# Kernel tuning notes

Measured on AMD Instinct MI355X. Metric: run time of the kernel, lower is better.

## Reference

```python
import jax
import jax.numpy as jnp
import numpy as np
from jax import lax

B, T, D = 32, 256, 512   # batch, seq len, controller_dim (== memory_dim)
S = 2048                 # memory_slots
EPS_LN = 1e-5            # nn.LayerNorm default eps
EPS_NRM = 1e-12          # F.normalize default eps


def setup_inputs() -> dict:
    key = jax.random.key(0)
    ks = jax.random.split(key, 12)
    sc = 1.0 / np.sqrt(D)  # roughly torch Linear init scale
    return {
        "controller_seq": jax.random.normal(ks[0], (B, T, D), dtype=jnp.float32),
        "memory": jax.random.normal(ks[1], (S, D), dtype=jnp.float32),
        "Wk": jax.random.normal(ks[2], (D, D), dtype=jnp.float32) * sc,
        "bk": jax.random.normal(ks[3], (D,), dtype=jnp.float32) * sc,
        "We": jax.random.normal(ks[4], (D, D), dtype=jnp.float32) * sc,
        "be": jax.random.normal(ks[5], (D,), dtype=jnp.float32) * sc,
        "Ww": jax.random.normal(ks[6], (D, D), dtype=jnp.float32) * sc,
        "bw": jax.random.normal(ks[7], (D,), dtype=jnp.float32) * sc,
        "Wg": jax.random.normal(ks[8], (D, D), dtype=jnp.float32) * sc,
        "bg": jax.random.normal(ks[9], (D,), dtype=jnp.float32) * sc,
        "gamma": jnp.ones((D,), dtype=jnp.float32),
        "beta": jnp.zeros((D,), dtype=jnp.float32),
    }


def _l2norm(x, axis=-1):
    # matches F.normalize: x / max(||x||, eps)
    n = jnp.sqrt(jnp.sum(x * x, axis=axis, keepdims=True))
    return x / jnp.maximum(n, EPS_NRM)


def _layernorm(x, gamma, beta):
    mu = jnp.mean(x, axis=-1, keepdims=True)
    var = jnp.mean((x - mu) ** 2, axis=-1, keepdims=True)
    return (x - mu) * lax.rsqrt(var + EPS_LN) * gamma + beta


def reference(controller_seq, memory, Wk, bk, We, be, Ww, bw, Wg, bg, gamma, beta):
    batch = controller_seq.shape[0]

    def step(mem, c):  # mem: [S, Dm], c: [B, Dc]
        # --- read (addressing by cosine similarity) ---
        k = c @ Wk.T + bk                       # [B, Dm]
        sim = _l2norm(k) @ _l2norm(mem).T       # [B, S]
        w = jax.nn.softmax(sim, axis=-1)        # [B, S]
        read_val = w @ mem                      # [B, Dm]
        # --- write (erase / add, averaged over batch) ---
        erase = jax.nn.sigmoid(c @ We.T + be)   # [B, Dm]
        add = c @ Ww.T + bw                     # [B, Dm]
        # mean_b (1 - w_bs * e_bd) = 1 - (w^T e)/B ; avoids [B,S,Dm] intermediate
        erase_m = 1.0 - jnp.einsum("bs,bd->sd", w, erase) / batch
        add_m = jnp.einsum("bs,bd->sd", w, add) / batch
        new_mem = _layernorm(mem * erase_m + add_m, gamma, beta)  # dropout in eval mode
        # --- gated output ---
        g = jax.nn.sigmoid(c @ Wg.T + bg)       # [B, Dm]
        out_t = g * c + (1.0 - g) * read_val
        return new_mem, out_t

    _, outs = lax.scan(step, memory, jnp.swapaxes(controller_seq, 0, 1))  # outs: [T, B, D]
    return jnp.swapaxes(outs, 0, 1)  # [B, T, D]
```

## Files before the change

### kernel.cpp

```cpp
#include <hip/hip_runtime.h>

#define DEV __device__ __forceinline__

namespace {
constexpr int Bc = 32;
constexpr int Tc = 256;
constexpr int Dc = 512;
constexpr int Sc = 2048;
constexpr int NBLK = 256;
constexpr int NW   = 128;
constexpr int ROWS = Sc / NW;

constexpr size_t OFF_KN  = 0;
constexpr size_t OFF_E   = OFF_KN  + (size_t)Tc * Bc * Dc;
constexpr size_t OFF_A   = OFF_E   + (size_t)Tc * Bc * Dc;
constexpr size_t OFF_MEM = OFF_A   + (size_t)Tc * Bc * Dc;
constexpr size_t OFF_EW  = OFF_MEM + (size_t)2 * Sc * Dc;
constexpr size_t OFF_RP  = OFF_EW  + (size_t)2 * Sc * Bc;
constexpr size_t OFF_DEN = OFF_RP  + (size_t)2 * 16 * Bc * Dc;
constexpr size_t OFF_CNT = OFF_DEN + (size_t)Tc * Bc;
}

DEV float sigm(float x) { return 1.0f / (1.0f + __expf(-x)); }

DEV float ld1cg(const float* p) {
  unsigned u = __hip_atomic_load((const unsigned*)p, __ATOMIC_RELAXED,
                                 __HIP_MEMORY_SCOPE_AGENT);
  return __uint_as_float(u);
}
DEV void st1cg(float* p, float v) {
  __hip_atomic_store((unsigned*)p, __float_as_uint(v), __ATOMIC_RELAXED,
                     __HIP_MEMORY_SCOPE_AGENT);
}
DEV float2 ld2cg(const float* p) {
  unsigned long long u = __hip_atomic_load((const unsigned long long*)p,
                                           __ATOMIC_RELAXED, __HIP_MEMORY_SCOPE_AGENT);
  union { unsigned long long u; float2 f; } c; c.u = u; return c.f;
}
DEV void st2cg(float* p, float2 v) {
  union { float2 f; unsigned long long u; } c; c.f = v;
  __hip_atomic_store((unsigned long long*)p, c.u, __ATOMIC_RELAXED,
                     __HIP_MEMORY_SCOPE_AGENT);
}

__global__ __launch_bounds__(256) void k_gemm(
    const float* __restrict__ A,
    const float* __restrict__ Wk, const float* __restrict__ bk,
    const float* __restrict__ We, const float* __restrict__ be,
    const float* __restrict__ Ww, const float* __restrict__ bw,
    const float* __restrict__ Wg, const float* __restrict__ bg,
    float* __restrict__ ws, float* __restrict__ gout)
{
  __shared__ float As[32][68];
  __shared__ float Bs[32][68];

  const int bid = blockIdx.x;
  const int mat = bid >> 10;
  const int rem = bid & 1023;
  const int rt = rem >> 3, jt = rem & 7;
  const int rbase = rt * 64, jbase = jt * 64;

  const float* Wm; const float* bm;
  if      (mat == 0) { Wm = Wk; bm = bk; }
  else if (mat == 1) { Wm = We; bm = be; }
  else if (mat == 2) { Wm = Ww; bm = bw; }
  else               { Wm = Wg; bm = bg; }

  const int tid = threadIdx.x;
  const int lr = tid >> 2;
  const int lk = (tid & 3) * 8;
  const int ty = tid >> 4, tx = tid & 15;

  float acc[4][4] = {};

  for (int k0 = 0; k0 < Dc; k0 += 32) {
    const float4 a0 = *(const float4*)&A [(size_t)(rbase + lr) * Dc + k0 + lk];
    const float4 a1 = *(const float4*)&A [(size_t)(rbase + lr) * Dc + k0 + lk + 4];
    const float4 b0 = *(const float4*)&Wm[(size_t)(jbase + lr) * Dc + k0 + lk];
    const float4 b1 = *(const float4*)&Wm[(size_t)(jbase + lr) * Dc + k0 + lk + 4];
    __syncthreads();
    As[lk + 0][lr] = a0.x; As[lk + 1][lr] = a0.y; As[lk + 2][lr] = a0.z; As[lk + 3][lr] = a0.w;
    As[lk + 4][lr] = a1.x; As[lk + 5][lr] = a1.y; As[lk + 6][lr] = a1.z; As[lk + 7][lr] = a1.w;
    Bs[lk + 0][lr] = b0.x; Bs[lk + 1][lr] = b0.y; Bs[lk + 2][lr] = b0.z; Bs[lk + 3][lr] = b0.w;
    Bs[lk + 4][lr] = b1.x; Bs[lk + 5][lr] = b1.y; Bs[lk + 6][lr] = b1.z; Bs[lk + 7][lr] = b1.w;
    __syncthreads();
    #pragma unroll
    for (int kk = 0; kk < 32; ++kk) {
      const float4 av = *(const float4*)&As[kk][ty * 4];
      const float4 bv = *(const float4*)&Bs[kk][tx * 4];
      const float ar[4] = {av.x, av.y, av.z, av.w};
      const float br[4] = {bv.x, bv.y, bv.z, bv.w};
      #pragma unroll
      for (int i = 0; i < 4; ++i)
        #pragma unroll
        for (int j = 0; j < 4; ++j)
          acc[i][j] = fmaf(ar[i], br[j], acc[i][j]);
    }
  }

  const float4 bias = *(const float4*)&bm[jbase + tx * 4];
  const float bi[4] = {bias.x, bias.y, bias.z, bias.w};
  #pragma unroll
  for (int i = 0; i < 4; ++i) {
    const int r = rbase + ty * 4 + i;
    float v[4];
    #pragma unroll
    for (int j = 0; j < 4; ++j) {
      v[j] = acc[i][j] + bi[j];
      if (mat & 1) v[j] = sigm(v[j]);
    }
    float4 o; o.x = v[0]; o.y = v[1]; o.z = v[2]; o.w = v[3];
    if (mat == 3) {
      *(float4*)&gout[(size_t)r * Dc + jbase + tx * 4] = o;
    } else {
      float* dst = ws + (mat == 0 ? OFF_KN : (mat == 1 ? OFF_E : OFF_A));
      const int t = r & 255, b = r >> 8;
      *(float4*)&dst[((size_t)t * Bc + b) * Dc + jbase + tx * 4] = o;
    }
  }
}

__global__ __launch_bounds__(256) void k_knorm(float* __restrict__ kn)
{
  const int row = blockIdx.x * 4 + (threadIdx.x >> 6);
  const int lane = threadIdx.x & 63;
  float* p = kn + (size_t)row * Dc;
  float4 v0 = *(const float4*)&p[lane * 4];
  float4 v1 = *(const float4*)&p[256 + lane * 4];
  float ss = v0.x*v0.x + v0.y*v0.y + v0.z*v0.z + v0.w*v0.w
           + v1.x*v1.x + v1.y*v1.y + v1.z*v1.z + v1.w*v1.w;
  #pragma unroll
  for (int off = 32; off >= 1; off >>= 1) ss += __shfl_xor(ss, off);
  const float inv = 1.0f / fmaxf(sqrtf(ss), 1e-12f);
  v0.x *= inv; v0.y *= inv; v0.z *= inv; v0.w *= inv;
  v1.x *= inv; v1.y *= inv; v1.z *= inv; v1.w *= inv;
  *(float4*)&p[lane * 4] = v0;
  *(float4*)&p[256 + lane * 4] = v1;
}

DEV void sim_phase(const float* __restrict__ knp, float* __restrict__ ewn,
                   float* __restrict__ denp, float (*xb)[516],
                   const float* invn_s, float* sred, int s0, int tid)
{
  const int r = tid >> 4, bp = tid & 15;
  const float* k0p = knp + (size_t)bp * Dc;
  const float* k1p = knp + (size_t)(bp + 16) * Dc;
  float acc0 = 0.f, acc1 = 0.f;
  #pragma unroll 4
  for (int dq = 0; dq < Dc / 4; ++dq) {
    const float4 y4 = *(const float4*)&xb[r][dq * 4];
    const float4 ka = *(const float4*)&k0p[dq * 4];
    const float4 kb = *(const float4*)&k1p[dq * 4];
    acc0 = fmaf(y4.x, ka.x, acc0); acc0 = fmaf(y4.y, ka.y, acc0);
    acc0 = fmaf(y4.z, ka.z, acc0); acc0 = fmaf(y4.w, ka.w, acc0);
    acc1 = fmaf(y4.x, kb.x, acc1); acc1 = fmaf(y4.y, kb.y, acc1);
    acc1 = fmaf(y4.z, kb.z, acc1); acc1 = fmaf(y4.w, kb.w, acc1);
  }
  const float iv = invn_s[r];
  const float e0 = __expf(acc0 * iv);
  const float e1 = __expf(acc1 * iv);
  st1cg(&ewn[(size_t)(s0 + r) * Bc + bp], e0);
  st1cg(&ewn[(size_t)(s0 + r) * Bc + bp + 16], e1);
  if (tid < 32) sred[tid] = 0.f;
  __syncthreads();
  atomicAdd(&sred[bp], e0);
  atomicAdd(&sred[bp + 16], e1);
  __syncthreads();
  if (tid < 32) atomicAdd(&denp[tid], sred[tid]);
}

__global__ __launch_bounds__(256) void k_prologue(
    const float* __restrict__ mem_in, float* __restrict__ ws)
{
  __shared__ float xbuf[16][516];
  __shared__ float sred[32];
  __shared__ float invn_s[16];

  float* kn   = ws + OFF_KN;
  float* memb = ws + OFF_MEM;
  float* ewb  = ws + OFF_EW;
  float* den  = ws + OFF_DEN;

  const int bid = blockIdx.x, tid = threadIdx.x;
  const int s0 = bid * ROWS;
  const int c0 = tid * 2;
  #pragma unroll
  for (int r = 0; r < ROWS; ++r) {
    const float2 m = *(const float2*)&mem_in[(size_t)(s0 + r) * Dc + c0];
    *(float2*)&xbuf[r][c0] = m;
    st2cg(&memb[(size_t)(s0 + r) * Dc + c0], m);
  }
  __syncthreads();
  {
    const int row = tid >> 4, li = tid & 15;
    float ss = 0.f;
    #pragma unroll
    for (int i = 0; i < 8; ++i) {
      const float4 v = *(const float4*)&xbuf[row][(li + i * 16) * 4];
      ss += v.x*v.x + v.y*v.y + v.z*v.z + v.w*v.w;
    }
    ss += __shfl_xor(ss, 8); ss += __shfl_xor(ss, 4);
    ss += __shfl_xor(ss, 2); ss += __shfl_xor(ss, 1);
    if (li == 0) invn_s[row] = 1.0f / fmaxf(sqrtf(ss), 1e-12f);
  }
  __syncthreads();
  sim_phase(kn, ewb, den, xbuf, invn_s, sred, s0, tid);
}

DEV void gbar(unsigned* cnt, unsigned target)
{
  __syncthreads();
  if (threadIdx.x == 0) {
    __hip_atomic_fetch_add(cnt, 1u, __ATOMIC_RELAXED, __HIP_MEMORY_SCOPE_AGENT);
    unsigned v = __hip_atomic_load(cnt, __ATOMIC_RELAXED, __HIP_MEMORY_SCOPE_AGENT);
    while (v < target) {
      __builtin_amdgcn_s_sleep(2);
      v = __hip_atomic_load(cnt, __ATOMIC_RELAXED, __HIP_MEMORY_SCOPE_AGENT);
    }
  }
  __syncthreads();
}

__global__ __launch_bounds__(256) void k_main(
    const float* __restrict__ cs,
    const float* __restrict__ gamma, const float* __restrict__ beta,
    float* __restrict__ ws, float* __restrict__ out)
{
  __shared__ float xbuf[16][516];
  __shared__ float wbuf[16][32];
  __shared__ float sred[32];
  __shared__ float mu_s[16], rs_s[16], invn_s[16];
  __shared__ float dinv_s[32];

  float* kn   = ws + OFF_KN;
  float* eptb = ws + OFF_E;
  float* aptb = ws + OFF_A;
  float* memb = ws + OFF_MEM;
  float* ewb  = ws + OFF_EW;
  float* rp   = ws + OFF_RP;
  float* den  = ws + OFF_DEN;
  unsigned* cnt = (unsigned*)(ws + OFF_CNT);

  const int bid = blockIdx.x, tid = threadIdx.x;
  const float inv32 = 1.0f / 32.0f;
  unsigned bart = 0;

  for (int t = 0; t <= Tc; ++t) {
    if (bid < NW) {
      if (t < Tc - 1) {
        const int s0 = bid * ROWS;
        const int c0 = tid * 2;
        const float* ewc = ewb + (size_t)(t & 1) * Sc * Bc;
        float*       ewn = ewb + (size_t)((t + 1) & 1) * Sc * Bc;
        const float* memc = memb + (size_t)(t & 1) * Sc * Dc;
        float*       memn = memb + (size_t)((t + 1) & 1) * Sc * Dc;

        if (tid < 32) dinv_s[tid] = 1.0f / ld1cg(&den[(size_t)t * Bc + tid]);
        __syncthreads();
        for (int idx = tid; idx < ROWS * 32; idx += 256) {
          const int r = idx >> 5, b = idx & 31;
          wbuf[r][b] = ld1cg(&ewc[(size_t)(s0 + r) * Bc + b]) * dinv_s[b];
        }
        __syncthreads();

        float2 er[ROWS] = {}, ad[ROWS] = {};
        const float* ept = eptb + (size_t)t * Bc * Dc;
        const float* apt = aptb + (size_t)t * Bc * Dc;
        #pragma unroll 4
        for (int b = 0; b < 32; ++b) {
          const float2 ev = *(const float2*)&ept[(size_t)b * Dc + c0];
          const float2 av = *(const float2*)&apt[(size_t)b * Dc + c0];
          #pragma unroll
          for (int r = 0; r < ROWS; ++r) {
            const float wv = wbuf[r][b];
            er[r].x = fmaf(wv, ev.x, er[r].x); er[r].y = fmaf(wv, ev.y, er[r].y);
            ad[r].x = fmaf(wv, av.x, ad[r].x); ad[r].y = fmaf(wv, av.y, ad[r].y);
          }
        }
        float2 xr[ROWS];
        #pragma unroll
        for (int r = 0; r < ROWS; ++r) {
          const float2 m = ld2cg(&memc[(size_t)(s0 + r) * Dc + c0]);
          float2 x;
          x.x = m.x * (1.0f - er[r].x * inv32) + ad[r].x * inv32;
          x.y = m.y * (1.0f - er[r].y * inv32) + ad[r].y * inv32;
          xr[r] = x;
          *(float2*)&xbuf[r][c0] = x;
        }
        __syncthreads();
        {
          const int row = tid >> 4, li = tid & 15;
          float s1 = 0.f, s2 = 0.f;
          #pragma unroll
          for (int i = 0; i < 8; ++i) {
            const float4 v = *(const float4*)&xbuf[row][(li + i * 16) * 4];
            s1 += v.x + v.y + v.z + v.w;
            s2 += v.x*v.x + v.y*v.y + v.z*v.z + v.w*v.w;
          }
          s1 += __shfl_xor(s1, 8); s2 += __shfl_xor(s2, 8);
          s1 += __shfl_xor(s1, 4); s2 += __shfl_xor(s2, 4);
          s1 += __shfl_xor(s1, 2); s2 += __shfl_xor(s2, 2);
          s1 += __shfl_xor(s1, 1); s2 += __shfl_xor(s2, 1);
          if (li == 0) {
            const float mu = s1 * (1.0f / 512.0f);
            const float var = s2 * (1.0f / 512.0f) - mu * mu;
            mu_s[row] = mu;
            rs_s[row] = rsqrtf(var + 1e-5f);
          }
        }
        __syncthreads();
        const float2 gm  = *(const float2*)&gamma[c0];
        const float2 bt2 = *(const float2*)&beta[c0];
        #pragma unroll
        for (int r = 0; r < ROWS; ++r) {
          const float mu = mu_s[r], rs = rs_s[r];
          float2 y;
          y.x = (xr[r].x - mu) * rs * gm.x + bt2.x;
          y.y = (xr[r].y - mu) * rs * gm.y + bt2.y;
          *(float2*)&xbuf[r][c0] = y;
          st2cg(&memn[(size_t)(s0 + r) * Dc + c0], y);
        }
        __syncthreads();
        {
          const int row = tid >> 4, li = tid & 15;
          float ss = 0.f;
          #pragma unroll
          for (int i = 0; i < 8; ++i) {
            const float4 v = *(const float4*)&xbuf[row][(li + i * 16) * 4];
            ss += v.x*v.x + v.y*v.y + v.z*v.z + v.w*v.w;
          }
          ss += __shfl_xor(ss, 8); ss += __shfl_xor(ss, 4);
          ss += __shfl_xor(ss, 2); ss += __shfl_xor(ss, 1);
          if (li == 0) invn_s[row] = 1.0f / fmaxf(sqrtf(ss), 1e-12f);
        }
        __syncthreads();
        sim_phase(kn + (size_t)(t + 1) * Bc * Dc, ewn,
                  den + (size_t)(t + 1) * Bc, xbuf, invn_s, sred, s0, tid);
      }
    } else {
      const int rb = bid - NW;
      if (rb < 8 && t >= 1) {
        const int t0 = t - 1;
        const float* rpc = rp + (size_t)(t0 & 1) * 16 * Bc * Dc;
        const int base = (rb * 256 + tid) * 8;
        const int b = base >> 9, d0 = base & 511;
        const float inv = 1.0f / ld1cg(&den[(size_t)t0 * Bc + b]);
        float r0[8] = {};
        #pragma unroll
        for (int si = 0; si < 16; ++si) {
          const float* q = rpc + ((size_t)si * Bc + b) * Dc + d0;
          const float2 p0 = ld2cg(q + 0);
          const float2 p1 = ld2cg(q + 2);
          const float2 p2 = ld2cg(q + 4);
          const float2 p3 = ld2cg(q + 6);
          r0[0] += p0.x; r0[1] += p0.y; r0[2] += p1.x; r0[3] += p1.y;
          r0[4] += p2.x; r0[5] += p2.y; r0[6] += p3.x; r0[7] += p3.y;
        }
        const size_t oofs = ((size_t)b * Tc + t0) * Dc + d0;
        const float4 g0 = *(const float4*)&out[oofs];
        const float4 g1 = *(const float4*)&out[oofs + 4];
        const float4 c0v = *(const float4*)&cs[oofs];
        const float4 c1v = *(const float4*)&cs[oofs + 4];
        float4 o0, o1;
        o0.x = g0.x * c0v.x + (1.0f - g0.x) * (r0[0] * inv);
        o0.y = g0.y * c0v.y + (1.0f - g0.y) * (r0[1] * inv);
        o0.z = g0.z * c0v.z + (1.0f - g0.z) * (r0[2] * inv);
        o0.w = g0.w * c0v.w + (1.0f - g0.w) * (r0[3] * inv);
        o1.x = g1.x * c1v.x + (1.0f - g1.x) * (r0[4] * inv);
        o1.y = g1.y * c1v.y + (1.0f - g1.y) * (r0[5] * inv);
        o1.z = g1.z * c1v.z + (1.0f - g1.z) * (r0[6] * inv);
        o1.w = g1.w * c1v.w + (1.0f - g1.w) * (r0[7] * inv);
        *(float4*)&out[oofs] = o0;
        *(float4*)&out[oofs + 4] = o1;
      }
      if (t < Tc) {
        const int si = rb >> 3, dj = rb & 7;
        const int sB = si * 128;
        const float* ewc = ewb + (size_t)(t & 1) * Sc * Bc;
        const float* memc = memb + (size_t)(t & 1) * Sc * Dc;
        float* ewl = (float*)xbuf;
        for (int i = tid; i < 128 * 32; i += 256)
          ewl[i] = ld1cg(&ewc[(size_t)sB * Bc + i]);
        __syncthreads();
        const int b = tid >> 3, dg = tid & 7;
        const int cbase = dj * 64 + dg * 8;
        float a0[8] = {};
        #pragma unroll 2
        for (int s = 0; s < 128; ++s) {
          const float wv = ewl[s * 32 + b];
          const float* mrow = memc + (size_t)(sB + s) * Dc + cbase;
          const float2 m0 = ld2cg(mrow + 0);
          const float2 m1 = ld2cg(mrow + 2);
          const float2 m2 = ld2cg(mrow + 4);
          const float2 m3 = ld2cg(mrow + 6);
          a0[0] = fmaf(wv, m0.x, a0[0]); a0[1] = fmaf(wv, m0.y, a0[1]);
          a0[2] = fmaf(wv, m1.x, a0[2]); a0[3] = fmaf(wv, m1.y, a0[3]);
          a0[4] = fmaf(wv, m2.x, a0[4]); a0[5] = fmaf(wv, m2.y, a0[5]);
          a0[6] = fmaf(wv, m3.x, a0[6]); a0[7] = fmaf(wv, m3.y, a0[7]);
        }
        float* dst = rp + (size_t)(t & 1) * 16 * Bc * Dc + ((size_t)si * Bc + b) * Dc + cbase;
        float2 w0; w0.x = a0[0]; w0.y = a0[1]; st2cg(dst + 0, w0);
        float2 w1; w1.x = a0[2]; w1.y = a0[3]; st2cg(dst + 2, w1);
        float2 w2; w2.x = a0[4]; w2.y = a0[5]; st2cg(dst + 4, w2);
        float2 w3; w3.x = a0[6]; w3.y = a0[7]; st2cg(dst + 6, w3);
        __syncthreads();
      }
    }
    if (t < Tc) { bart += NBLK; gbar(cnt, bart); }
  }
}

extern "C" void kernel_launch(void* const* d_in, const int* in_sizes, int n_in,
                              void* d_out, int out_size, void* d_ws, size_t ws_size,
                              hipStream_t stream)
{
  const float* cs    = (const float*)d_in[0];
  const float* mem   = (const float*)d_in[1];
  const float* Wk    = (const float*)d_in[2];
  const float* bk    = (const float*)d_in[3];
  const float* We    = (const float*)d_in[4];
  const float* be    = (const float*)d_in[5];
  const float* Ww    = (const float*)d_in[6];
  const float* bw    = (const float*)d_in[7];
  const float* Wg    = (const float*)d_in[8];
  const float* bg    = (const float*)d_in[9];
  const float* gamma = (const float*)d_in[10];
  const float* beta  = (const float*)d_in[11];
  float* ws  = (float*)d_ws;
  float* out = (float*)d_out;

  hipMemsetAsync(ws + OFF_DEN, 0, ((size_t)Tc * Bc + 1) * sizeof(float), stream);

  hipLaunchKernelGGL(k_gemm, dim3(4096), dim3(256), 0, stream,
                     cs, Wk, bk, We, be, Ww, bw, Wg, bg, ws, out);
  hipLaunchKernelGGL(k_knorm, dim3(2048), dim3(256), 0, stream, ws + OFF_KN);
  hipLaunchKernelGGL(k_prologue, dim3(NW), dim3(256), 0, stream, mem, ws);
  hipLaunchKernelGGL(k_main, dim3(NBLK), dim3(256), 0, stream,
                     cs, gamma, beta, ws, out);
}
```

Measured before the change: 12.15 ms.

## Replace atomic-counter grid barrier with flag/go barrier that aggregates softmax denominators

Replaces the single-counter grid barrier with per-block padded flags polled by block 0, which then releases a go flag. Block 0 also sums the per-block softmax partial denominators during the barrier, so the global float atomics on den are gone. Memory rows and exp-weights of each writer block stay in LDS across steps instead of being reloaded from global, and the prologue kernel is folded into k_main. A reader-loop unroll bump and one removed __syncthreads come along; in exchange block 0 serialises the barrier and LDS use per block grows.

```diff
diff --git a/kernel.cpp b/kernel.cpp
--- a/kernel.cpp
+++ b/kernel.cpp
@@ -11,14 +11,16 @@
 constexpr int NW   = 128;
 constexpr int ROWS = Sc / NW;
 
-constexpr size_t OFF_KN  = 0;
-constexpr size_t OFF_E   = OFF_KN  + (size_t)Tc * Bc * Dc;
-constexpr size_t OFF_A   = OFF_E   + (size_t)Tc * Bc * Dc;
-constexpr size_t OFF_MEM = OFF_A   + (size_t)Tc * Bc * Dc;
-constexpr size_t OFF_EW  = OFF_MEM + (size_t)2 * Sc * Dc;
-constexpr size_t OFF_RP  = OFF_EW  + (size_t)2 * Sc * Bc;
-constexpr size_t OFF_DEN = OFF_RP  + (size_t)2 * 16 * Bc * Dc;
-constexpr size_t OFF_CNT = OFF_DEN + (size_t)Tc * Bc;
+constexpr size_t OFF_KN   = 0;
+constexpr size_t OFF_E    = OFF_KN  + (size_t)Tc * Bc * Dc;
+constexpr size_t OFF_A    = OFF_E   + (size_t)Tc * Bc * Dc;
+constexpr size_t OFF_MEM  = OFF_A   + (size_t)Tc * Bc * Dc;
+constexpr size_t OFF_EW   = OFF_MEM + (size_t)2 * Sc * Dc;
+constexpr size_t OFF_RP   = OFF_EW  + (size_t)2 * Sc * Bc;
+constexpr size_t OFF_DEN  = OFF_RP  + (size_t)2 * 16 * Bc * Dc;
+constexpr size_t OFF_DENP = OFF_DEN + (size_t)Tc * Bc;
+constexpr size_t OFF_FLAGS= OFF_DENP+ (size_t)2 * NW * Bc;
+constexpr size_t OFF_GO   = OFF_FLAGS + 256 * 16;
 }
 
 DEV float sigm(float x) { return 1.0f / (1.0f + __expf(-x)); }
@@ -138,8 +140,50 @@
   *(float4*)&p[256 + lane * 4] = v1;
 }
 
+DEV void gbar(unsigned* flags, unsigned* go, unsigned step, int bid, int tid,
+              int do_agg, const float* denp_par, float* den_out, float* lds_red)
+{
+  __syncthreads();
+  if (bid == 0) {
+    if (tid > 0) {
+      while (__hip_atomic_load(&flags[tid * 16], __ATOMIC_RELAXED,
+                               __HIP_MEMORY_SCOPE_AGENT) < step)
+        __builtin_amdgcn_s_sleep(2);
+    }
+    __syncthreads();
+    if (do_agg) {
+      const int b = tid & 31, ch = tid >> 5;
+      float s = 0.f;
+      #pragma unroll
+      for (int g = 0; g < 16; ++g)
+        s += ld1cg(&denp_par[(size_t)(ch * 16 + g) * Bc + b]);
+      lds_red[tid] = s;
+      __syncthreads();
+      if (tid < 32) {
+        float tot = 0.f;
+        #pragma unroll
+        for (int c2 = 0; c2 < 8; ++c2) tot += lds_red[c2 * 32 + tid];
+        st1cg(&den_out[tid], tot);
+      }
+    }
+    __syncthreads();
+    if (tid == 0)
+      __hip_atomic_store(go, step, __ATOMIC_RELAXED, __HIP_MEMORY_SCOPE_AGENT);
+  } else {
+    if (tid == 0) {
+      __hip_atomic_store(&flags[bid * 16], step, __ATOMIC_RELAXED,
+                         __HIP_MEMORY_SCOPE_AGENT);
+      while (__hip_atomic_load(go, __ATOMIC_RELAXED,
+                               __HIP_MEMORY_SCOPE_AGENT) < step)
+        __builtin_amdgcn_s_sleep(2);
+    }
+    __syncthreads();
+  }
+}
+
 DEV void sim_phase(const float* __restrict__ knp, float* __restrict__ ewn,
-                   float* __restrict__ denp, float (*xb)[516],
+                   float* __restrict__ denp_row, const float (*y)[516],
+                   float* __restrict__ ew_own,
                    const float* invn_s, float* sred, int s0, int tid)
 {
   const int r = tid >> 4, bp = tid & 15;
@@ -148,7 +192,7 @@
   float acc0 = 0.f, acc1 = 0.f;
   #pragma unroll 4
   for (int dq = 0; dq < Dc / 4; ++dq) {
-    const float4 y4 = *(const float4*)&xb[r][dq * 4];
+    const float4 y4 = *(const float4*)&y[r][dq * 4];
     const float4 ka = *(const float4*)&k0p[dq * 4];
     const float4 kb = *(const float4*)&k1p[dq * 4];
     acc0 = fmaf(y4.x, ka.x, acc0); acc0 = fmaf(y4.y, ka.y, acc0);
@@ -161,76 +205,28 @@
   const float e1 = __expf(acc1 * iv);
   st1cg(&ewn[(size_t)(s0 + r) * Bc + bp], e0);
   st1cg(&ewn[(size_t)(s0 + r) * Bc + bp + 16], e1);
+  ew_own[r * 32 + bp]      = e0;
+  ew_own[r * 32 + bp + 16] = e1;
   if (tid < 32) sred[tid] = 0.f;
   __syncthreads();
   atomicAdd(&sred[bp], e0);
   atomicAdd(&sred[bp + 16], e1);
   __syncthreads();
-  if (tid < 32) atomicAdd(&denp[tid], sred[tid]);
-}
-
-__global__ __launch_bounds__(256) void k_prologue(
-    const float* __restrict__ mem_in, float* __restrict__ ws)
-{
-  __shared__ float xbuf[16][516];
-  __shared__ float sred[32];
-  __shared__ float invn_s[16];
-
-  float* kn   = ws + OFF_KN;
-  float* memb = ws + OFF_MEM;
-  float* ewb  = ws + OFF_EW;
-  float* den  = ws + OFF_DEN;
-
-  const int bid = blockIdx.x, tid = threadIdx.x;
-  const int s0 = bid * ROWS;
-  const int c0 = tid * 2;
-  #pragma unroll
-  for (int r = 0; r < ROWS; ++r) {
-    const float2 m = *(const float2*)&mem_in[(size_t)(s0 + r) * Dc + c0];
-    *(float2*)&xbuf[r][c0] = m;
-    st2cg(&memb[(size_t)(s0 + r) * Dc + c0], m);
-  }
-  __syncthreads();
-  {
-    const int row = tid >> 4, li = tid & 15;
-    float ss = 0.f;
-    #pragma unroll
-    for (int i = 0; i < 8; ++i) {
-      const float4 v = *(const float4*)&xbuf[row][(li + i * 16) * 4];
-      ss += v.x*v.x + v.y*v.y + v.z*v.z + v.w*v.w;
-    }
-    ss += __shfl_xor(ss, 8); ss += __shfl_xor(ss, 4);
-    ss += __shfl_xor(ss, 2); ss += __shfl_xor(ss, 1);
-    if (li == 0) invn_s[row] = 1.0f / fmaxf(sqrtf(ss), 1e-12f);
-  }
-  __syncthreads();
-  sim_phase(kn, ewb, den, xbuf, invn_s, sred, s0, tid);
-}
-
-DEV void gbar(unsigned* cnt, unsigned target)
-{
-  __syncthreads();
-  if (threadIdx.x == 0) {
-    __hip_atomic_fetch_add(cnt, 1u, __ATOMIC_RELAXED, __HIP_MEMORY_SCOPE_AGENT);
-    unsigned v = __hip_atomic_load(cnt, __ATOMIC_RELAXED, __HIP_MEMORY_SCOPE_AGENT);
-    while (v < target) {
-      __builtin_amdgcn_s_sleep(2);
-      v = __hip_atomic_load(cnt, __ATOMIC_RELAXED, __HIP_MEMORY_SCOPE_AGENT);
-    }
-  }
-  __syncthreads();
+  if (tid < 32) st1cg(&denp_row[tid], sred[tid]);
 }
 
 __global__ __launch_bounds__(256) void k_main(
-    const float* __restrict__ cs,
+    const float* __restrict__ cs, const float* __restrict__ mem_in,
     const float* __restrict__ gamma, const float* __restrict__ beta,
     float* __restrict__ ws, float* __restrict__ out)
 {
+  __shared__ float mrows[16][516];
   __shared__ float xbuf[16][516];
+  __shared__ float ew_own[16 * 32];
   __shared__ float wbuf[16][32];
+  __shared__ float lds_red[256];
   __shared__ float sred[32];
-  __shared__ float mu_s[16], rs_s[16], invn_s[16];
-  __shared__ float dinv_s[32];
+  __shared__ float mu_s[16], rs_s[16], invn_s[16], dinv_s[32];
 
   float* kn   = ws + OFF_KN;
   float* eptb = ws + OFF_E;
@@ -239,28 +235,54 @@
   float* ewb  = ws + OFF_EW;
   float* rp   = ws + OFF_RP;
   float* den  = ws + OFF_DEN;
-  unsigned* cnt = (unsigned*)(ws + OFF_CNT);
+  float* denp = ws + OFF_DENP;
+  unsigned* flags = (unsigned*)(ws + OFF_FLAGS);
+  unsigned* go    = (unsigned*)(ws + OFF_GO);
 
   const int bid = blockIdx.x, tid = threadIdx.x;
   const float inv32 = 1.0f / 32.0f;
-  unsigned bart = 0;
+
+  if (bid < NW) {
+    const int s0 = bid * ROWS;
+    const int c0 = tid * 2;
+    #pragma unroll
+    for (int r = 0; r < ROWS; ++r) {
+      const float2 m = *(const float2*)&mem_in[(size_t)(s0 + r) * Dc + c0];
+      *(float2*)&mrows[r][c0] = m;
+      st2cg(&memb[(size_t)(s0 + r) * Dc + c0], m);
+    }
+    __syncthreads();
+    {
+      const int row = tid >> 4, li = tid & 15;
+      float ss = 0.f;
+      #pragma unroll
+      for (int i = 0; i < 8; ++i) {
+        const float4 v = *(const float4*)&mrows[row][(li + i * 16) * 4];
+        ss += v.x*v.x + v.y*v.y + v.z*v.z + v.w*v.w;
+      }
+      ss += __shfl_xor(ss, 8); ss += __shfl_xor(ss, 4);
+      ss += __shfl_xor(ss, 2); ss += __shfl_xor(ss, 1);
+      if (li == 0) invn_s[row] = 1.0f / fmaxf(sqrtf(ss), 1e-12f);
+    }
+    __syncthreads();
+    sim_phase(kn, ewb, denp + (size_t)bid * Bc, mrows, ew_own,
+              invn_s, sred, s0, tid);
+  }
+  gbar(flags, go, 1u, bid, tid, 1, denp, den, lds_red);
 
   for (int t = 0; t <= Tc; ++t) {
     if (bid < NW) {
       if (t < Tc - 1) {
         const int s0 = bid * ROWS;
         const int c0 = tid * 2;
-        const float* ewc = ewb + (size_t)(t & 1) * Sc * Bc;
-        float*       ewn = ewb + (size_t)((t + 1) & 1) * Sc * Bc;
-        const float* memc = memb + (size_t)(t & 1) * Sc * Dc;
-        float*       memn = memb + (size_t)((t + 1) & 1) * Sc * Dc;
+        float* ewn  = ewb  + (size_t)((t + 1) & 1) * Sc * Bc;
+        float* memn = memb + (size_t)((t + 1) & 1) * Sc * Dc;
+        float* denp_n = denp + (size_t)((t + 1) & 1) * NW * Bc + (size_t)bid * Bc;
 
         if (tid < 32) dinv_s[tid] = 1.0f / ld1cg(&den[(size_t)t * Bc + tid]);
         __syncthreads();
-        for (int idx = tid; idx < ROWS * 32; idx += 256) {
-          const int r = idx >> 5, b = idx & 31;
-          wbuf[r][b] = ld1cg(&ewc[(size_t)(s0 + r) * Bc + b]) * dinv_s[b];
-        }
+        for (int idx = tid; idx < ROWS * 32; idx += 256)
+          wbuf[idx >> 5][idx & 31] = ew_own[idx] * dinv_s[idx & 31];
         __syncthreads();
 
         float2 er[ROWS] = {}, ad[ROWS] = {};
@@ -280,7 +302,7 @@
         float2 xr[ROWS];
         #pragma unroll
         for (int r = 0; r < ROWS; ++r) {
-          const float2 m = ld2cg(&memc[(size_t)(s0 + r) * Dc + c0]);
+          const float2 m = *(const float2*)&mrows[r][c0];
           float2 x;
           x.x = m.x * (1.0f - er[r].x * inv32) + ad[r].x * inv32;
           x.y = m.y * (1.0f - er[r].y * inv32) + ad[r].y * inv32;
@@ -317,7 +339,7 @@
           float2 y;
           y.x = (xr[r].x - mu) * rs * gm.x + bt2.x;
           y.y = (xr[r].y - mu) * rs * gm.y + bt2.y;
-          *(float2*)&xbuf[r][c0] = y;
+          *(float2*)&mrows[r][c0] = y;
           st2cg(&memn[(size_t)(s0 + r) * Dc + c0], y);
         }
         __syncthreads();
@@ -326,7 +348,7 @@
           float ss = 0.f;
           #pragma unroll
           for (int i = 0; i < 8; ++i) {
-            const float4 v = *(const float4*)&xbuf[row][(li + i * 16) * 4];
+            const float4 v = *(const float4*)&mrows[row][(li + i * 16) * 4];
             ss += v.x*v.x + v.y*v.y + v.z*v.z + v.w*v.w;
           }
           ss += __shfl_xor(ss, 8); ss += __shfl_xor(ss, 4);
@@ -334,8 +356,8 @@
           if (li == 0) invn_s[row] = 1.0f / fmaxf(sqrtf(ss), 1e-12f);
         }
         __syncthreads();
-        sim_phase(kn + (size_t)(t + 1) * Bc * Dc, ewn,
-                  den + (size_t)(t + 1) * Bc, xbuf, invn_s, sred, s0, tid);
+        sim_phase(kn + (size_t)(t + 1) * Bc * Dc, ewn, denp_n, mrows, ew_own,
+                  invn_s, sred, s0, tid);
       }
     } else {
       const int rb = bid - NW;
@@ -385,7 +407,7 @@
         const int b = tid >> 3, dg = tid & 7;
         const int cbase = dj * 64 + dg * 8;
         float a0[8] = {};
-        #pragma unroll 2
+        #pragma unroll 4
         for (int s = 0; s < 128; ++s) {
           const float wv = ewl[s * 32 + b];
           const float* mrow = memc + (size_t)(sB + s) * Dc + cbase;
@@ -403,10 +425,14 @@
         float2 w1; w1.x = a0[2]; w1.y = a0[3]; st2cg(dst + 2, w1);
         float2 w2; w2.x = a0[4]; w2.y = a0[5]; st2cg(dst + 4, w2);
         float2 w3; w3.x = a0[6]; w3.y = a0[7]; st2cg(dst + 6, w3);
-        __syncthreads();
       }
     }
-    if (t < Tc) { bart += NBLK; gbar(cnt, bart); }
+    if (t < Tc) {
+      const int do_agg = (t + 1 < Tc) ? 1 : 0;
+      gbar(flags, go, (unsigned)(t + 2), bid, tid, do_agg,
+           denp + (size_t)((t + 1) & 1) * NW * Bc,
+           den + (size_t)(t + 1) * Bc, lds_red);
+    }
   }
 }
 
@@ -429,12 +455,11 @@
   float* ws  = (float*)d_ws;
   float* out = (float*)d_out;
 
-  hipMemsetAsync(ws + OFF_DEN, 0, ((size_t)Tc * Bc + 1) * sizeof(float), stream);
+  hipMemsetAsync(ws + OFF_FLAGS, 0, (256 * 16 + 1) * sizeof(unsigned), stream);
 
   hipLaunchKernelGGL(k_gemm, dim3(4096), dim3(256), 0, stream,
                      cs, Wk, bk, We, be, Ww, bw, Wg, bg, ws, out);
   hipLaunchKernelGGL(k_knorm, dim3(2048), dim3(256), 0, stream, ws + OFF_KN);
-  hipLaunchKernelGGL(k_prologue, dim3(NW), dim3(256), 0, stream, mem, ws);
   hipLaunchKernelGGL(k_main, dim3(NBLK), dim3(256), 0, stream,
-                     cs, gamma, beta, ws, out);
-}
+                     cs, mem, gamma, beta, ws, out);
+}
```

Result: no change. 12.12 ms (-0.2%).
